# Performance work log

Hardware: AMD Instinct MI355X
Metric: run time of the kernel (lower is better)

The kernel has to match this reference:

```python
import jax, jax.numpy as jnp
import numpy as np

TEMP = 8.0  # softmax temperature from softmax_(X, N=8.0)
EPS = 1e-12  # F.normalize eps


def qmul(q, r):
    # Hamilton product, quaternions stored as (w, x, y, z); broadcasts over leading dims.
    w1, x1, y1, z1 = q[..., 0], q[..., 1], q[..., 2], q[..., 3]
    w2, x2, y2, z2 = r[..., 0], r[..., 1], r[..., 2], r[..., 3]
    return jnp.stack([
        w1 * w2 - x1 * x2 - y1 * y2 - z1 * z2,
        w1 * x2 + x1 * w2 + y1 * z2 - z1 * y2,
        w1 * y2 - x1 * z2 + y1 * w2 + z1 * x2,
        w1 * z2 + x1 * y2 - y1 * x2 + z1 * w2,
    ], axis=-1)


def setup_inputs() -> dict:
    key = jax.random.key(0)
    kl, kq, krq, kw, ks, kd = jax.random.split(key, 6)
    N, K, E = 100000, 8, 3200000
    node_levels = jax.random.uniform(kl, (N, K), dtype=jnp.float32)
    node_q = jax.random.normal(kq, (N, K, 4), dtype=jnp.float32)
    node_q = node_q / jnp.linalg.norm(node_q, axis=-1, keepdims=True)
    edge_rel_q = jax.random.normal(krq, (E, 4), dtype=jnp.float32)
    edge_rel_q = edge_rel_q / jnp.linalg.norm(edge_rel_q, axis=-1, keepdims=True)
    edge_w = jax.random.uniform(kw, (E,), dtype=jnp.float32)
    edge_src = jax.random.randint(ks, (E,), 0, N, dtype=jnp.int32)
    edge_dst = jax.random.randint(kd, (E,), 0, N, dtype=jnp.int32)
    return {"node_levels": node_levels, "node_q": node_q, "edge_rel_q": edge_rel_q,
            "edge_w": edge_w, "edge_src": edge_src, "edge_dst": edge_dst}


def reference(node_levels, node_q, edge_rel_q, edge_w, edge_src, edge_dst):
    N, K = node_levels.shape
    # --- gather (DGL message_func): per-edge source features ---
    q_src = node_q[edge_src]          # [E,K,4]
    l_src = node_levels[edge_src]     # [E,K]
    # accumulated quaternion: rel_q (broadcast over K) * neighbor q
    accu_q = qmul(edge_rel_q[:, None, :], q_src)  # [E,K,4]

    # --- distance-weighted softmax over {self} U in-neighbors, per (node, k) ---
    score_e = TEMP * edge_w[:, None] * l_src      # [E,K]  edge term: w * l
    score_s = TEMP * node_levels                  # [N,K]  self term: w=1
    seg_max = jax.ops.segment_max(score_e, edge_dst, num_segments=N)  # -inf if no in-edges
    m = jnp.maximum(seg_max, score_s)             # [N,K] stable max incl. self
    exp_e = jnp.exp(score_e - m[edge_dst])
    exp_s = jnp.exp(score_s - m)
    denom = jax.ops.segment_sum(exp_e, edge_dst, num_segments=N) + exp_s  # [N,K]
    w_e = exp_e / denom[edge_dst]                 # [E,K]
    w_s = exp_s / denom                           # [N,K]

    # --- weighted aggregation (scatter) ---
    out_q = jax.ops.segment_sum(w_e[..., None] * accu_q, edge_dst, num_segments=N) \
            + w_s[..., None] * node_q             # [N,K,4]
    out_levels = jax.ops.segment_sum(w_e * l_src, edge_dst, num_segments=N) \
            + w_s * node_levels                   # [N,K]

    # F.normalize(p=2, dim=-1) with eps clamp
    norm = jnp.maximum(jnp.linalg.norm(out_q, axis=-1, keepdims=True), EPS)
    q = out_q / norm
    return q, out_levels
```

## Files before the change

kernel.cpp:

```cpp
#include <hip/hip_runtime.h>
#include <hip/hip_fp16.h>

#define TEMP 8.0f
#define MSHIFT 8.0f
#define KDIM 8

__device__ __forceinline__ unsigned pack_h2(float a, float b) {
    __half2 h = __floats2half2_rn(a, b);
    return __builtin_bit_cast(unsigned, h);
}
__device__ __forceinline__ float2 unpack_h2(unsigned v) {
    __half2 h = __builtin_bit_cast(__half2, v);
    return __half22float2(h);
}

__global__ void nodepack(const float* __restrict__ levels,
                         const float4* __restrict__ node_q,
                         float4* __restrict__ packed, int NK) {
    int i = blockIdx.x * blockDim.x + threadIdx.x;
    if (i >= NK) return;
    float4 q = node_q[i];
    uint4 u;
    u.x = pack_h2(q.x, q.y);
    u.y = pack_h2(q.z, q.w);
    u.z = __builtin_bit_cast(unsigned, levels[i]);
    u.w = 0;
    packed[i] = __builtin_bit_cast(float4, u);
}

__global__ void bucket_scatter(const int* __restrict__ edst,
                               const int* __restrict__ esrc,
                               const float* __restrict__ ew,
                               const float4* __restrict__ rel_q,
                               int* __restrict__ deg,
                               float4* __restrict__ payload,
                               int CAP, int E) {
    int e = blockIdx.x * blockDim.x + threadIdx.x;
    if (e >= E) return;
    int dst = edst[e];
    int pos = atomicAdd(&deg[dst], 1);
    if (pos >= CAP) return;
    float4 r = rel_q[e];
    uint4 u;
    u.x = pack_h2(r.x, r.y);
    u.y = pack_h2(r.z, r.w);
    u.z = __builtin_bit_cast(unsigned, TEMP * ew[e]);
    u.w = (unsigned)(esrc[e] * KDIM);
    payload[(size_t)dst * CAP + pos] = __builtin_bit_cast(float4, u);
}

__global__ void agg_bucket(const float* __restrict__ levels,
                           const float4* __restrict__ node_q,
                           const float4* __restrict__ packed,
                           const int* __restrict__ deg,
                           const float4* __restrict__ payload,
                           int CAP,
                           float4* __restrict__ out_q,
                           float* __restrict__ out_lvl, int N) {
    int t = blockIdx.x * blockDim.x + threadIdx.x;
    int n = t >> 3;
    int k = t & 7;
    if (n >= N) return;
    int i = n * KDIM + k;

    float l = levels[i];
    float es = __expf(TEMP * l - MSHIFT);
    float den = es, lv = es * l;
    float4 q0 = node_q[i];
    float aw = es * q0.x, ax = es * q0.y, ay = es * q0.z, az = es * q0.w;

    int cnt = deg[n];
    if (cnt > CAP) cnt = CAP;
    const float4* bp = payload + (size_t)n * CAP;
#pragma unroll 4
    for (int j = 0; j < cnt; j++) {
        float4 pe = bp[j];
        uint4 pu = __builtin_bit_cast(uint4, pe);
        float2 r01 = unpack_h2(pu.x);
        float2 r23 = unpack_h2(pu.y);
        float tw = pe.z;
        int src8 = (int)pu.w;
        float4 nd = packed[src8 + k];
        uint4 nu = __builtin_bit_cast(uint4, nd);
        float2 q01 = unpack_h2(nu.x);
        float2 q23 = unpack_h2(nu.y);
        float ls = nd.z;
        float ex = __expf(tw * ls - MSHIFT);
        den += ex;
        lv += ex * ls;
        float rw = r01.x, rx = r01.y, ry = r23.x, rz = r23.y;
        float qw = q01.x, qx = q01.y, qy = q23.x, qz = q23.y;
        aw += ex * (rw * qw - rx * qx - ry * qy - rz * qz);
        ax += ex * (rw * qx + rx * qw + ry * qz - rz * qy);
        ay += ex * (rw * qy - rx * qz + ry * qw + rz * qx);
        az += ex * (rw * qz + rx * qy - ry * qx + rz * qw);
    }

    float inv = 1.0f / den;
    lv *= inv; aw *= inv; ax *= inv; ay *= inv; az *= inv;
    float nn = sqrtf(aw * aw + ax * ax + ay * ay + az * az);
    nn = fmaxf(nn, 1e-12f);
    float rn = 1.0f / nn;
    float4 o;
    o.x = aw * rn; o.y = ax * rn; o.z = ay * rn; o.w = az * rn;
    out_q[i] = o;
    out_lvl[i] = lv;
}


__global__ void rank_kernel(const int* __restrict__ edst, int* __restrict__ deg,
                            int* __restrict__ rank, int E) {
    int e = blockIdx.x * blockDim.x + threadIdx.x;
    if (e < E) rank[e] = atomicAdd(&deg[edst[e]], 1);
}

__global__ void scan1(const int* __restrict__ deg, int* __restrict__ offs,
                      int* __restrict__ bsum, int N) {
    __shared__ int s[256];
    int i = blockIdx.x * 256 + threadIdx.x;
    int v = (i < N) ? deg[i] : 0;
    s[threadIdx.x] = v;
    __syncthreads();
    for (int off = 1; off < 256; off <<= 1) {
        int t = (threadIdx.x >= off) ? s[threadIdx.x - off] : 0;
        __syncthreads();
        s[threadIdx.x] += t;
        __syncthreads();
    }
    if (i < N) offs[i] = s[threadIdx.x] - v;
    if (threadIdx.x == 255) bsum[blockIdx.x] = s[255];
}

__global__ void scan2(int* __restrict__ bsum, int nb) {
    __shared__ int s[1024];
    __shared__ int carry_s;
    if (threadIdx.x == 0) carry_s = 0;
    __syncthreads();
    for (int base = 0; base < nb; base += 1024) {
        int idx = base + threadIdx.x;
        int v = (idx < nb) ? bsum[idx] : 0;
        s[threadIdx.x] = v;
        __syncthreads();
        for (int off = 1; off < 1024; off <<= 1) {
            int t = (threadIdx.x >= off) ? s[threadIdx.x - off] : 0;
            __syncthreads();
            s[threadIdx.x] += t;
            __syncthreads();
        }
        if (idx < nb) bsum[idx] = s[threadIdx.x] - v + carry_s;
        __syncthreads();
        if (threadIdx.x == 0) carry_s += s[1023];
        __syncthreads();
    }
}

__global__ void scan3(int* __restrict__ offs, const int* __restrict__ bsum,
                      int N, int E) {
    int i = blockIdx.x * 256 + threadIdx.x;
    if (i < N) offs[i] += bsum[blockIdx.x];
    if (i == 0) offs[N] = E;
}

__global__ void permute_kernel(const int* __restrict__ edst,
                               const int* __restrict__ rank,
                               const int* __restrict__ offs,
                               const float4* __restrict__ rel_q,
                               const float* __restrict__ ew,
                               const int* __restrict__ esrc,
                               float4* __restrict__ payload, int E) {
    int e = blockIdx.x * blockDim.x + threadIdx.x;
    if (e >= E) return;
    int pos = offs[edst[e]] + rank[e];
    payload[2 * pos] = rel_q[e];
    float4 m;
    m.x = TEMP * ew[e];
    m.y = __int_as_float(esrc[e] * KDIM);
    m.z = 0.0f; m.w = 0.0f;
    payload[2 * pos + 1] = m;
}

__global__ void agg_payload(const float* __restrict__ levels,
                            const float4* __restrict__ node_q,
                            const int* __restrict__ offs,
                            const float4* __restrict__ payload,
                            float4* __restrict__ out_q,
                            float* __restrict__ out_lvl, int N) {
    int t = blockIdx.x * blockDim.x + threadIdx.x;
    int n = t >> 3;
    int k = t & 7;
    if (n >= N) return;
    int i = n * KDIM + k;
    float l = levels[i];
    float es = __expf(TEMP * l - MSHIFT);
    float den = es, lv = es * l;
    float4 q0 = node_q[i];
    float aw = es * q0.x, ax = es * q0.y, ay = es * q0.z, az = es * q0.w;
    int beg = offs[n], end = offs[n + 1];
#pragma unroll 2
    for (int j = beg; j < end; j++) {
        float4 r = payload[2 * j];
        float4 m = payload[2 * j + 1];
        float tw = m.x;
        int src8 = __float_as_int(m.y);
        float ls = levels[src8 + k];
        float ex = __expf(tw * ls - MSHIFT);
        float4 q = node_q[src8 + k];
        den += ex;
        lv += ex * ls;
        aw += ex * (r.x * q.x - r.y * q.y - r.z * q.z - r.w * q.w);
        ax += ex * (r.x * q.y + r.y * q.x + r.z * q.w - r.w * q.z);
        ay += ex * (r.x * q.z - r.y * q.w + r.z * q.x + r.w * q.y);
        az += ex * (r.x * q.w + r.y * q.z - r.z * q.y + r.w * q.x);
    }
    float inv = 1.0f / den;
    lv *= inv; aw *= inv; ax *= inv; ay *= inv; az *= inv;
    float nn = sqrtf(aw * aw + ax * ax + ay * ay + az * az);
    nn = fmaxf(nn, 1e-12f);
    float rn = 1.0f / nn;
    float4 o;
    o.x = aw * rn; o.y = ax * rn; o.z = ay * rn; o.w = az * rn;
    out_q[i] = o;
    out_lvl[i] = lv;
}

extern "C" void kernel_launch(void* const* d_in, const int* in_sizes, int n_in,
                              void* d_out, int out_size, void* d_ws, size_t ws_size,
                              hipStream_t stream) {
    const float*  levels = (const float*)d_in[0];
    const float4* node_q = (const float4*)d_in[1];
    const float4* rel_q  = (const float4*)d_in[2];
    const float*  ew     = (const float*)d_in[3];
    const int*    esrc   = (const int*)d_in[4];
    const int*    edst   = (const int*)d_in[5];

    const int NK = in_sizes[0];
    const int E  = in_sizes[3];
    const int N  = NK / KDIM;
    const int B  = 256;
    const int gE = (E + B - 1) / B;
    const int gN = (NK + B - 1) / B;

    float* out_q   = (float*)d_out;
    float* out_lvl = (float*)d_out + (size_t)NK * 4;

    size_t deg_bytes  = ((size_t)N * 4 + 255) & ~(size_t)255;
    size_t pack_bytes = (size_t)NK * 16;
    long long cap_avail = 0;
    if (ws_size > deg_bytes + pack_bytes)
        cap_avail = (long long)((ws_size - deg_bytes - pack_bytes) / ((size_t)N * 16));
    int CAP = (cap_avail > 96) ? 96 : (int)cap_avail;

    if (CAP >= 80) {
        int* deg = (int*)d_ws;
        float4* packed  = (float4*)((char*)d_ws + deg_bytes);
        float4* payload = (float4*)((char*)d_ws + deg_bytes + pack_bytes);
        hipMemsetAsync(deg, 0, (size_t)N * sizeof(int), stream);
        nodepack<<<gN, B, 0, stream>>>(levels, node_q, packed, NK);
        bucket_scatter<<<gE, B, 0, stream>>>(edst, esrc, ew, rel_q, deg, payload,
                                             CAP, E);
        agg_bucket<<<gN, B, 0, stream>>>(levels, node_q, packed, deg, payload, CAP,
                                         (float4*)out_q, out_lvl, N);
        return;
    }

    const int nb = (N + 255) / 256;
    int* deg  = (int*)d_ws;
    int* offs = deg + N;
    int* bsum = offs + N + 1;
    size_t prefix = (size_t)(2 * N + 1 + nb);
    int* rank = bsum + nb;
    size_t pay_off = (prefix + E + 3) & ~(size_t)3;
    float4* payload = (float4*)((int*)d_ws + pay_off);

    hipMemsetAsync(deg, 0, (size_t)N * sizeof(int), stream);
    rank_kernel<<<gE, B, 0, stream>>>(edst, deg, rank, E);
    scan1<<<nb, 256, 0, stream>>>(deg, offs, bsum, N);
    scan2<<<1, 1024, 0, stream>>>(bsum, nb);
    scan3<<<nb, 256, 0, stream>>>(offs, bsum, N, E);
    permute_kernel<<<gE, B, 0, stream>>>(edst, rank, offs, rel_q, ew, esrc,
                                         payload, E);
    agg_payload<<<gN, B, 0, stream>>>(levels, node_q, offs, payload,
                                      (float4*)out_q, out_lvl, N);
}
```

Baseline: 348.6 us.

## Split node table into fp16 quats plus levels, add nontemporal payload access

Replaces the 16-byte packed node record (fp16 quaternion, level, padding) with a separate 8-byte fp16 quaternion array, and reads levels straight from the input array. This removes the padding word from the gather and shrinks the node-pack pass. Payload stores in the bucket scatter and payload loads in the aggregation now use nontemporal hints, and the aggregation loop unroll goes from 4 to 8. The trade-off is two gather loads per edge instead of one, which may cost more transactions than the bytes saved.

```diff
diff --git a/kernel.cpp b/kernel.cpp
--- a/kernel.cpp
+++ b/kernel.cpp
@@ -5,6 +5,8 @@
 #define MSHIFT 8.0f
 #define KDIM 8
 
+typedef float nfloat4 __attribute__((ext_vector_type(4)));
+
 __device__ __forceinline__ unsigned pack_h2(float a, float b) {
     __half2 h = __floats2half2_rn(a, b);
     return __builtin_bit_cast(unsigned, h);
@@ -14,18 +16,15 @@
     return __half22float2(h);
 }
 
-__global__ void nodepack(const float* __restrict__ levels,
-                         const float4* __restrict__ node_q,
-                         float4* __restrict__ packed, int NK) {
+__global__ void nodepack8(const float4* __restrict__ node_q,
+                          uint2* __restrict__ q16, int NK) {
     int i = blockIdx.x * blockDim.x + threadIdx.x;
     if (i >= NK) return;
     float4 q = node_q[i];
-    uint4 u;
+    uint2 u;
     u.x = pack_h2(q.x, q.y);
     u.y = pack_h2(q.z, q.w);
-    u.z = __builtin_bit_cast(unsigned, levels[i]);
-    u.w = 0;
-    packed[i] = __builtin_bit_cast(float4, u);
+    q16[i] = u;
 }
 
 __global__ void bucket_scatter(const int* __restrict__ edst,
@@ -46,12 +45,13 @@
     u.y = pack_h2(r.z, r.w);
     u.z = __builtin_bit_cast(unsigned, TEMP * ew[e]);
     u.w = (unsigned)(esrc[e] * KDIM);
-    payload[(size_t)dst * CAP + pos] = __builtin_bit_cast(float4, u);
+    nfloat4 v = __builtin_bit_cast(nfloat4, u);
+    __builtin_nontemporal_store(v, (nfloat4*)&payload[(size_t)dst * CAP + pos]);
 }
 
 __global__ void agg_bucket(const float* __restrict__ levels,
                            const float4* __restrict__ node_q,
-                           const float4* __restrict__ packed,
+                           const uint2* __restrict__ q16,
                            const int* __restrict__ deg,
                            const float4* __restrict__ payload,
                            int CAP,
@@ -71,20 +71,19 @@
 
     int cnt = deg[n];
     if (cnt > CAP) cnt = CAP;
-    const float4* bp = payload + (size_t)n * CAP;
-#pragma unroll 4
+    const nfloat4* bp = (const nfloat4*)(payload + (size_t)n * CAP);
+#pragma unroll 8
     for (int j = 0; j < cnt; j++) {
-        float4 pe = bp[j];
+        nfloat4 pe = __builtin_nontemporal_load(&bp[j]);
         uint4 pu = __builtin_bit_cast(uint4, pe);
         float2 r01 = unpack_h2(pu.x);
         float2 r23 = unpack_h2(pu.y);
-        float tw = pe.z;
+        float tw = __builtin_bit_cast(float, pu.z);
         int src8 = (int)pu.w;
-        float4 nd = packed[src8 + k];
-        uint4 nu = __builtin_bit_cast(uint4, nd);
-        float2 q01 = unpack_h2(nu.x);
-        float2 q23 = unpack_h2(nu.y);
-        float ls = nd.z;
+        uint2 qu = q16[src8 + k];
+        float ls = levels[src8 + k];
+        float2 q01 = unpack_h2(qu.x);
+        float2 q23 = unpack_h2(qu.y);
         float ex = __expf(tw * ls - MSHIFT);
         den += ex;
         lv += ex * ls;
@@ -244,21 +243,21 @@
     float* out_lvl = (float*)d_out + (size_t)NK * 4;
 
     size_t deg_bytes  = ((size_t)N * 4 + 255) & ~(size_t)255;
-    size_t pack_bytes = (size_t)NK * 16;
+    size_t q16_bytes  = ((size_t)NK * 8 + 255) & ~(size_t)255;
     long long cap_avail = 0;
-    if (ws_size > deg_bytes + pack_bytes)
-        cap_avail = (long long)((ws_size - deg_bytes - pack_bytes) / ((size_t)N * 16));
+    if (ws_size > deg_bytes + q16_bytes)
+        cap_avail = (long long)((ws_size - deg_bytes - q16_bytes) / ((size_t)N * 16));
     int CAP = (cap_avail > 96) ? 96 : (int)cap_avail;
 
     if (CAP >= 80) {
         int* deg = (int*)d_ws;
-        float4* packed  = (float4*)((char*)d_ws + deg_bytes);
-        float4* payload = (float4*)((char*)d_ws + deg_bytes + pack_bytes);
-        hipMemsetAsync(deg, 0, (size_t)N * sizeof(int), stream);
-        nodepack<<<gN, B, 0, stream>>>(levels, node_q, packed, NK);
+        uint2* q16      = (uint2*)((char*)d_ws + deg_bytes);
+        float4* payload = (float4*)((char*)d_ws + deg_bytes + q16_bytes);
+        (void)hipMemsetAsync(deg, 0, (size_t)N * sizeof(int), stream);
+        nodepack8<<<gN, B, 0, stream>>>(node_q, q16, NK);
         bucket_scatter<<<gE, B, 0, stream>>>(edst, esrc, ew, rel_q, deg, payload,
                                              CAP, E);
-        agg_bucket<<<gN, B, 0, stream>>>(levels, node_q, packed, deg, payload, CAP,
+        agg_bucket<<<gN, B, 0, stream>>>(levels, node_q, q16, deg, payload, CAP,
                                          (float4*)out_q, out_lvl, N);
         return;
     }
@@ -272,7 +271,7 @@
     size_t pay_off = (prefix + E + 3) & ~(size_t)3;
     float4* payload = (float4*)((int*)d_ws + pay_off);
 
-    hipMemsetAsync(deg, 0, (size_t)N * sizeof(int), stream);
+    (void)hipMemsetAsync(deg, 0, (size_t)N * sizeof(int), stream);
     rank_kernel<<<gE, B, 0, stream>>>(edst, deg, rank, E);
     scan1<<<nb, 256, 0, stream>>>(deg, offs, bsum, N);
     scan2<<<1, 1024, 0, stream>>>(bsum, nb);
```

Result: slower. 504.1 us (+44.6%).

## Assign one wavefront per node, splitting its edge list across 8 lane groups

Applied to the files above, without the earlier changes.

The bucket aggregation kernel now gives each node a full 64-lane wavefront instead of 8 lanes. Eight segments of 8 lanes each stride through the node's incoming edges, and partial sums are combined with xor shuffles before the self term and normalization are applied. The aim is to shorten the serial per-node edge loop (about 32 edges on average) and expose more memory-level parallelism. In exchange it launches 8x more threads, leaves many lanes idle on low-degree nodes, and adds shuffle reduction work.

```diff
diff --git a/kernel.cpp b/kernel.cpp
--- a/kernel.cpp
+++ b/kernel.cpp
@@ -49,37 +49,34 @@
     payload[(size_t)dst * CAP + pos] = __builtin_bit_cast(float4, u);
 }
 
-__global__ void agg_bucket(const float* __restrict__ levels,
-                           const float4* __restrict__ node_q,
-                           const float4* __restrict__ packed,
-                           const int* __restrict__ deg,
-                           const float4* __restrict__ payload,
-                           int CAP,
-                           float4* __restrict__ out_q,
-                           float* __restrict__ out_lvl, int N) {
+__global__ void agg_wave(const float* __restrict__ levels,
+                         const float4* __restrict__ node_q,
+                         const float4* __restrict__ packed,
+                         const int* __restrict__ deg,
+                         const float4* __restrict__ payload,
+                         int CAP,
+                         float4* __restrict__ out_q,
+                         float* __restrict__ out_lvl, int N) {
     int t = blockIdx.x * blockDim.x + threadIdx.x;
-    int n = t >> 3;
-    int k = t & 7;
+    int n = t >> 6;
     if (n >= N) return;
-    int i = n * KDIM + k;
-
-    float l = levels[i];
-    float es = __expf(TEMP * l - MSHIFT);
-    float den = es, lv = es * l;
-    float4 q0 = node_q[i];
-    float aw = es * q0.x, ax = es * q0.y, ay = es * q0.z, az = es * q0.w;
+    int lane = t & 63;
+    int k = lane & 7;
+    int seg = lane >> 3;
+
+    float den = 0.f, lv = 0.f, aw = 0.f, ax = 0.f, ay = 0.f, az = 0.f;
 
     int cnt = deg[n];
     if (cnt > CAP) cnt = CAP;
     const float4* bp = payload + (size_t)n * CAP;
-#pragma unroll 4
-    for (int j = 0; j < cnt; j++) {
+#pragma unroll 2
+    for (int j = seg; j < cnt; j += 8) {
         float4 pe = bp[j];
         uint4 pu = __builtin_bit_cast(uint4, pe);
         float2 r01 = unpack_h2(pu.x);
         float2 r23 = unpack_h2(pu.y);
         float tw = pe.z;
-        int src8 = (int)pu.w;
+        int src8 = __builtin_bit_cast(int, pu.w);
         float4 nd = packed[src8 + k];
         uint4 nu = __builtin_bit_cast(uint4, nd);
         float2 q01 = unpack_h2(nu.x);
@@ -96,15 +93,35 @@
         az += ex * (rw * qz + rx * qy - ry * qx + rz * qw);
     }
 
-    float inv = 1.0f / den;
-    lv *= inv; aw *= inv; ax *= inv; ay *= inv; az *= inv;
-    float nn = sqrtf(aw * aw + ax * ax + ay * ay + az * az);
-    nn = fmaxf(nn, 1e-12f);
-    float rn = 1.0f / nn;
-    float4 o;
-    o.x = aw * rn; o.y = ax * rn; o.z = ay * rn; o.w = az * rn;
-    out_q[i] = o;
-    out_lvl[i] = lv;
+#pragma unroll
+    for (int m = 8; m <= 32; m <<= 1) {
+        den += __shfl_xor(den, m, 64);
+        lv  += __shfl_xor(lv,  m, 64);
+        aw  += __shfl_xor(aw,  m, 64);
+        ax  += __shfl_xor(ax,  m, 64);
+        ay  += __shfl_xor(ay,  m, 64);
+        az  += __shfl_xor(az,  m, 64);
+    }
+
+    if (seg == 0) {
+        int i = n * KDIM + k;
+        float l = levels[i];
+        float es = __expf(TEMP * l - MSHIFT);
+        den += es;
+        lv += es * l;
+        float4 q0 = node_q[i];
+        aw += es * q0.x; ax += es * q0.y; ay += es * q0.z; az += es * q0.w;
+
+        float inv = 1.0f / den;
+        lv *= inv; aw *= inv; ax *= inv; ay *= inv; az *= inv;
+        float nn = sqrtf(aw * aw + ax * ax + ay * ay + az * az);
+        nn = fmaxf(nn, 1e-12f);
+        float rn = 1.0f / nn;
+        float4 o;
+        o.x = aw * rn; o.y = ax * rn; o.z = ay * rn; o.w = az * rn;
+        out_q[i] = o;
+        out_lvl[i] = lv;
+    }
 }
 
 
@@ -244,7 +261,7 @@
     float* out_lvl = (float*)d_out + (size_t)NK * 4;
 
     size_t deg_bytes  = ((size_t)N * 4 + 255) & ~(size_t)255;
-    size_t pack_bytes = (size_t)NK * 16;
+    size_t pack_bytes = ((size_t)NK * 16 + 255) & ~(size_t)255;
     long long cap_avail = 0;
     if (ws_size > deg_bytes + pack_bytes)
         cap_avail = (long long)((ws_size - deg_bytes - pack_bytes) / ((size_t)N * 16));
@@ -254,12 +271,13 @@
         int* deg = (int*)d_ws;
         float4* packed  = (float4*)((char*)d_ws + deg_bytes);
         float4* payload = (float4*)((char*)d_ws + deg_bytes + pack_bytes);
-        hipMemsetAsync(deg, 0, (size_t)N * sizeof(int), stream);
+        (void)hipMemsetAsync(deg, 0, (size_t)N * sizeof(int), stream);
         nodepack<<<gN, B, 0, stream>>>(levels, node_q, packed, NK);
         bucket_scatter<<<gE, B, 0, stream>>>(edst, esrc, ew, rel_q, deg, payload,
                                              CAP, E);
-        agg_bucket<<<gN, B, 0, stream>>>(levels, node_q, packed, deg, payload, CAP,
-                                         (float4*)out_q, out_lvl, N);
+        int gW = (int)(((size_t)N * 64 + B - 1) / B);
+        agg_wave<<<gW, B, 0, stream>>>(levels, node_q, packed, deg, payload, CAP,
+                                       (float4*)out_q, out_lvl, N);
         return;
     }
 
@@ -272,7 +290,7 @@
     size_t pay_off = (prefix + E + 3) & ~(size_t)3;
     float4* payload = (float4*)((int*)d_ws + pay_off);
 
-    hipMemsetAsync(deg, 0, (size_t)N * sizeof(int), stream);
+    (void)hipMemsetAsync(deg, 0, (size_t)N * sizeof(int), stream);
     rank_kernel<<<gE, B, 0, stream>>>(edst, deg, rank, E);
     scan1<<<nb, 256, 0, stream>>>(deg, offs, bsum, N);
     scan2<<<1, 1024, 0, stream>>>(bsum, nb);
```

Measured after the change: 337.3 us. 3.3% less time.
